# Optimization experiments

Measured on AMD Instinct MI355X. Metric: run time of the kernel, lower is better.

The kernel has to match this reference:

```python
import jax, jax.numpy as jnp
import numpy as np

N_NODES = 100000
N_EDGES = 6400000
ATOM_F = 128
R_CUT = 5.0


def setup_inputs() -> dict:
    key = jax.random.key(0)
    ks = jax.random.split(key, 9)
    x = jax.random.normal(ks[0], (N_NODES, ATOM_F), dtype=jnp.float32)
    rij = jax.random.uniform(ks[1], (N_EDGES,), dtype=jnp.float32) * R_CUT
    vij = jax.random.normal(ks[2], (N_EDGES, 3), dtype=jnp.float32)
    src = jax.random.randint(ks[3], (N_EDGES,), 0, N_NODES)
    dst = jax.random.randint(ks[4], (N_EDGES,), 0, N_NODES)
    # Dense params (PyTorch Linear default-ish init scale)
    s1 = 1.0 / np.sqrt(ATOM_F)
    W1 = jax.random.uniform(ks[5], (ATOM_F, ATOM_F), dtype=jnp.float32, minval=-s1, maxval=s1)
    b1 = jnp.zeros((ATOM_F,), dtype=jnp.float32)
    W2 = jax.random.uniform(ks[6], (ATOM_F, 1), dtype=jnp.float32, minval=-s1, maxval=s1)
    b2 = jnp.zeros((1,), dtype=jnp.float32)
    return {"x": x, "rij": rij, "vij": vij, "src": src, "dst": dst,
            "W1": W1, "b1": b1, "W2": W2, "b2": b2}


def reference(x, rij, vij, src, dst, W1, b1, W2, b2):
    # transform: Dense(F,F,swish) -> Dense(F,1,swish)
    h = jax.nn.silu(x @ W1 + b1)          # [N, F]
    q = jax.nn.silu(h @ W2 + b2)          # [N, 1]
    # cosine cutoff on edge distances
    c_ij = 0.5 * (jnp.cos(jnp.pi * rij / R_CUT) + 1.0)
    c_ij = c_ij * (rij < R_CUT).astype(rij.dtype)  # [E]
    # e_mul_u: broadcast source-node scalar onto edge vectors, scale by cutoff
    mu_ij = vij * q[src] * c_ij[:, None]  # [E, 3]
    # copy_e_sum: scatter-add edges into destination nodes
    mu = jax.ops.segment_sum(mu_ij, dst, num_segments=N_NODES)  # [N, 3]
    return mu
```

## Files before the change

### kernel.cpp

```cpp
#include <hip/hip_runtime.h>
#include <hip/hip_bf16.h>

#define NN 100000
#define NE 6400000
#define NSL 16
#define SLICE 6250
#define NB1 625
#define CHUNK (NE / NB1)
#define BCAP 840
#define C2 48
#define QSCALE 650.0f
#define QINV (1.0f / 650.0f)
#define QBIAS 5461

typedef __bf16 bf16x8_t __attribute__((ext_vector_type(8)));
typedef float f32x4_t __attribute__((ext_vector_type(4)));

__device__ __forceinline__ float silu_f(float v) { return v / (1.0f + __expf(-v)); }

__device__ __forceinline__ unsigned f16b(float v) {
    _Float16 h = (_Float16)v;
    unsigned short u;
    __builtin_memcpy(&u, &h, 2);
    return (unsigned)u;
}
__device__ __forceinline__ float f16f(unsigned u) {
    unsigned short us = (unsigned short)u;
    _Float16 h;
    __builtin_memcpy(&h, &us, 2);
    return (float)h;
}

__global__ __launch_bounds__(256, 2) void node_q_kernel(
    const float* __restrict__ x,
    const float* __restrict__ W1,
    const float* __restrict__ b1,
    const float* __restrict__ W2,
    const float* __restrict__ b2,
    float* __restrict__ q,
    int nGroups)
{
    __shared__ __align__(16) __bf16 w1s[2048 * 8];

    const int lane = threadIdx.x & 63;
    const int wave = threadIdx.x >> 6;
    const int c    = lane & 15;
    const int quad = lane >> 4;
    const int gwave  = blockIdx.x * 4 + wave;
    const int nWaves = gridDim.x * 4;

#pragma unroll
    for (int it = 0; it < 8; ++it) {
        const int e   = it * 256 + threadIdx.x;
        const int c_  = e & 15;
        const int nt_ = (e >> 4) & 7;
        const int qd  = (e >> 7) & 3;
        const int kt_ = e >> 9;
        const float* p = W1 + (kt_ * 32 + qd * 8) * 128 + nt_ * 16 + c_;
        bf16x8_t v;
#pragma unroll
        for (int j = 0; j < 8; ++j) v[j] = (__bf16)p[j * 128];
        *reinterpret_cast<bf16x8_t*>(&w1s[e * 8]) = v;
    }
    __syncthreads();

    bf16x8_t bfrag[8][4];
    float b1v[8], w2v[8];
#pragma unroll
    for (int nt = 0; nt < 8; ++nt) {
#pragma unroll
        for (int kt = 0; kt < 4; ++kt)
            bfrag[nt][kt] = *reinterpret_cast<const bf16x8_t*>(
                &w1s[(((kt * 4 + quad) * 8 + nt) * 16 + c) * 8]);
        b1v[nt] = b1[nt * 16 + c];
        w2v[nt] = W2[nt * 16 + c];
    }
    const float b2v = b2[0];

    for (int g = gwave; g < nGroups; g += nWaves) {
        const float* xrow = x + (size_t)(g * 16 + c) * 128 + quad * 8;
        bf16x8_t afrag[4];
#pragma unroll
        for (int kt = 0; kt < 4; ++kt) {
            const f32x4_t x0 = *reinterpret_cast<const f32x4_t*>(xrow + kt * 32);
            const f32x4_t x1 = *reinterpret_cast<const f32x4_t*>(xrow + kt * 32 + 4);
#pragma unroll
            for (int j = 0; j < 4; ++j) {
                afrag[kt][j]     = (__bf16)x0[j];
                afrag[kt][j + 4] = (__bf16)x1[j];
            }
        }

        float cr[4] = {0.f, 0.f, 0.f, 0.f};
#pragma unroll
        for (int nt = 0; nt < 8; ++nt) {
            f32x4_t acc = {0.f, 0.f, 0.f, 0.f};
#pragma unroll
            for (int kt = 0; kt < 4; ++kt)
                acc = __builtin_amdgcn_mfma_f32_16x16x32_bf16(afrag[kt], bfrag[nt][kt], acc, 0, 0, 0);
#pragma unroll
            for (int r = 0; r < 4; ++r)
                cr[r] += silu_f(acc[r] + b1v[nt]) * w2v[nt];
        }
#pragma unroll
        for (int r = 0; r < 4; ++r) {
            float v = cr[r];
            v += __shfl_xor(v, 1);
            v += __shfl_xor(v, 2);
            v += __shfl_xor(v, 4);
            v += __shfl_xor(v, 8);
            cr[r] = v;
        }
        if (c == 0) {
#pragma unroll
            for (int r = 0; r < 4; ++r)
                q[g * 16 + quad * 4 + r] = silu_f(cr[r] + b2v);
        }
    }
}

__global__ __launch_bounds__(256) void bucket_kernel(
    const float4* __restrict__ rij4,
    const float4* __restrict__ vij4,
    const int4* __restrict__ src4,
    const int4* __restrict__ dst4,
    const float* __restrict__ q,
    int* __restrict__ counts,
    uint2* __restrict__ arena)
{
    __shared__ int lcnt[NSL];
    const int t = threadIdx.x;
    const int lane = t & 63;
    if (t < NSL) lcnt[t] = 0;
    __syncthreads();

    const unsigned long long ltmask = (1ull << lane) - 1ull;
    const int g4 = blockIdx.x * (CHUNK / 4);
    const float K = 0.62831853071795864769f;

    for (int i = 0; i < CHUNK / 4 / 256; ++i) {
        const int idx = g4 + i * 256 + t;
        const int4 s = src4[idx];
        const int4 d = dst4[idx];
        const float4 r = rij4[idx];
        const float4 v0 = vij4[3 * idx + 0];
        const float4 v1 = vij4[3 * idx + 1];
        const float4 v2 = vij4[3 * idx + 2];

        const float c0 = (r.x < 5.0f) ? 0.5f * (__cosf(r.x * K) + 1.0f) : 0.0f;
        const float c1 = (r.y < 5.0f) ? 0.5f * (__cosf(r.y * K) + 1.0f) : 0.0f;
        const float c2 = (r.z < 5.0f) ? 0.5f * (__cosf(r.z * K) + 1.0f) : 0.0f;
        const float c3 = (r.w < 5.0f) ? 0.5f * (__cosf(r.w * K) + 1.0f) : 0.0f;
        const float w0 = q[s.x] * c0, w1 = q[s.y] * c1;
        const float w2 = q[s.z] * c2, w3 = q[s.w] * c3;

        int   dn[4] = {d.x, d.y, d.z, d.w};
        float px[4] = {v0.x * w0, v0.w * w1, v1.z * w2, v2.y * w3};
        float py[4] = {v0.y * w0, v1.x * w1, v1.w * w2, v2.z * w3};
        float pz[4] = {v0.z * w0, v1.y * w1, v2.x * w2, v2.w * w3};

#pragma unroll
        for (int j = 0; j < 4; ++j) {
            const int k  = dn[j] / SLICE;
            const int dl = dn[j] - k * SLICE;
            const float fx = fminf(fmaxf(px[j], -8.f), 8.f);
            const float fy = fminf(fmaxf(py[j], -8.f), 8.f);
            const float fz = fminf(fmaxf(pz[j], -8.f), 8.f);
            uint2 rec;
            rec.x = (unsigned)dl | (f16b(fx) << 16);
            rec.y = f16b(fy) | (f16b(fz) << 16);

            const unsigned long long b0 = __ballot(k & 1);
            const unsigned long long b1m = __ballot(k & 2);
            const unsigned long long b2m = __ballot(k & 4);
            const unsigned long long b3m = __ballot(k & 8);
            const unsigned long long eq =
                ((k & 1) ? b0 : ~b0) & ((k & 2) ? b1m : ~b1m) &
                ((k & 4) ? b2m : ~b2m) & ((k & 8) ? b3m : ~b3m);
            const int leader = __ffsll((long long)eq) - 1;
            const int rank   = __popcll(eq & ltmask);
            int base = 0;
            if (lane == leader) base = atomicAdd(&lcnt[k], __popcll(eq));
            base = __shfl(base, leader);
            const int pos = base + rank;
            if (pos < BCAP)
                arena[((size_t)k * NB1 + blockIdx.x) * BCAP + pos] = rec;
        }
    }
    __syncthreads();
    if (t < NSL) counts[blockIdx.x * NSL + t] = lcnt[t];
}

__global__ __launch_bounds__(256) void reduce_kernel(
    const uint2* __restrict__ arena,
    const int* __restrict__ counts,
    float* __restrict__ part)
{
    __shared__ unsigned long long acc[SLICE];
    const int s = blockIdx.x / C2;
    const int c = blockIdx.x % C2;

    for (int i = threadIdx.x; i < SLICE; i += 256) acc[i] = 0ull;
    __syncthreads();

    for (int b = c; b < NB1; b += C2) {
        const int n = counts[b * NSL + s];
        const uint2* seg = arena + ((size_t)s * NB1 + b) * BCAP;
        for (int i = threadIdx.x; i < n; i += 256) {
            const uint2 r = seg[i];
            const int node = r.x & 0xffffu;
            const int ix = __float2int_rn(f16f(r.x >> 16)      * QSCALE) + QBIAS;
            const int iy = __float2int_rn(f16f(r.y & 0xffffu)  * QSCALE) + QBIAS;
            const int iz = __float2int_rn(f16f(r.y >> 16)      * QSCALE) + QBIAS;
            const unsigned long long inc =
                (1ull << 54) |
                ((unsigned long long)(unsigned)ix << 36) |
                ((unsigned long long)(unsigned)iy << 18) |
                (unsigned long long)(unsigned)iz;
            atomicAdd(&acc[node], inc);
        }
    }
    __syncthreads();

    float* dp = part + (size_t)blockIdx.x * (SLICE * 3);
    for (int i = threadIdx.x; i < SLICE; i += 256) {
        const unsigned long long a = acc[i];
        const int cnt = (int)(a >> 54);
        const int X = (int)((a >> 36) & 0x3FFFFu) - cnt * QBIAS;
        const int Y = (int)((a >> 18) & 0x3FFFFu) - cnt * QBIAS;
        const int Z = (int)(a & 0x3FFFFu)         - cnt * QBIAS;
        dp[i * 3 + 0] = (float)X * QINV;
        dp[i * 3 + 1] = (float)Y * QINV;
        dp[i * 3 + 2] = (float)Z * QINV;
    }
}

__global__ __launch_bounds__(256) void finalize_kernel(
    const float* __restrict__ part,
    float* __restrict__ out)
{
    const int i = blockIdx.x * 256 + threadIdx.x;
    if (i >= NN * 3) return;
    const int n   = i / 3;
    const int k   = i - n * 3;
    const int s   = n / SLICE;
    const int l   = n - s * SLICE;
    const float* p = part + ((size_t)s * C2) * (SLICE * 3) + l * 3 + k;
    float sum = 0.f;
#pragma unroll
    for (int c = 0; c < C2; ++c) sum += p[(size_t)c * (SLICE * 3)];
    out[i] = sum;
}

__global__ __launch_bounds__(256) void edge_atomic_kernel(
    const float4* __restrict__ rij4,
    const float4* __restrict__ vij4,
    const int4* __restrict__ src4,
    const int4* __restrict__ dst4,
    const float* __restrict__ q,
    float* __restrict__ mu)
{
    const int t = blockIdx.x * 256 + threadIdx.x;
    const int4 s = src4[t];
    const int4 d = dst4[t];
    const float4 r = rij4[t];
    const float4 v0 = vij4[3 * t + 0];
    const float4 v1 = vij4[3 * t + 1];
    const float4 v2 = vij4[3 * t + 2];
    const float K = 0.62831853071795864769f;
    const float c0 = (r.x < 5.0f) ? 0.5f * (__cosf(r.x * K) + 1.0f) : 0.0f;
    const float c1 = (r.y < 5.0f) ? 0.5f * (__cosf(r.y * K) + 1.0f) : 0.0f;
    const float c2 = (r.z < 5.0f) ? 0.5f * (__cosf(r.z * K) + 1.0f) : 0.0f;
    const float c3 = (r.w < 5.0f) ? 0.5f * (__cosf(r.w * K) + 1.0f) : 0.0f;
    const float s0 = q[s.x] * c0, s1 = q[s.y] * c1, s2 = q[s.z] * c2, s3 = q[s.w] * c3;
    float* m0 = mu + 3 * (size_t)d.x;
    atomicAdd(m0 + 0, v0.x * s0); atomicAdd(m0 + 1, v0.y * s0); atomicAdd(m0 + 2, v0.z * s0);
    float* m1 = mu + 3 * (size_t)d.y;
    atomicAdd(m1 + 0, v0.w * s1); atomicAdd(m1 + 1, v1.x * s1); atomicAdd(m1 + 2, v1.y * s1);
    float* m2 = mu + 3 * (size_t)d.z;
    atomicAdd(m2 + 0, v1.z * s2); atomicAdd(m2 + 1, v1.w * s2); atomicAdd(m2 + 2, v2.x * s2);
    float* m3 = mu + 3 * (size_t)d.w;
    atomicAdd(m3 + 0, v2.y * s3); atomicAdd(m3 + 1, v2.z * s3); atomicAdd(m3 + 2, v2.w * s3);
}

extern "C" void kernel_launch(void* const* d_in, const int* in_sizes, int n_in,
                              void* d_out, int out_size, void* d_ws, size_t ws_size,
                              hipStream_t stream)
{
    const float* x   = (const float*)d_in[0];
    const float* rij = (const float*)d_in[1];
    const float* vij = (const float*)d_in[2];
    const int*   src = (const int*)d_in[3];
    const int*   dst = (const int*)d_in[4];
    const float* W1  = (const float*)d_in[5];
    const float* b1  = (const float*)d_in[6];
    const float* W2  = (const float*)d_in[7];
    const float* b2  = (const float*)d_in[8];

    char* ws = (char*)d_ws;
    const size_t Q_OFF    = 0;
    const size_t CNT_OFF  = 425984;
    const size_t REC_OFF  = 1048576;
    const size_t PART_OFF = REC_OFF + (size_t)NSL * NB1 * BCAP * 8;
    const size_t WS_NEEDED = PART_OFF + (size_t)NSL * C2 * SLICE * 3 * 4;

    float* q = (float*)(ws + Q_OFF);

    node_q_kernel<<<512, 256, 0, stream>>>(x, W1, b1, W2, b2, q, NN / 16);

    if (ws_size >= WS_NEEDED) {
        int*   counts = (int*)(ws + CNT_OFF);
        uint2* arena  = (uint2*)(ws + REC_OFF);
        float* part   = (float*)(ws + PART_OFF);

        bucket_kernel<<<NB1, 256, 0, stream>>>(
            (const float4*)rij, (const float4*)vij, (const int4*)src, (const int4*)dst,
            q, counts, arena);
        reduce_kernel<<<NSL * C2, 256, 0, stream>>>(arena, counts, part);
        finalize_kernel<<<(NN * 3 + 255) / 256, 256, 0, stream>>>(part, (float*)d_out);
    } else {
        hipMemsetAsync(d_out, 0, (size_t)NN * 3 * sizeof(float), stream);
        edge_atomic_kernel<<<NE / 4 / 256, 256, 0, stream>>>(
            (const float4*)rij, (const float4*)vij, (const int4*)src, (const int4*)dst,
            q, (float*)d_out);
    }
}
```

Measured before the change: 318.3 us.

## Stage bucketed edge records in LDS ring and flush in full wave-sized chunks

The bucketing kernel now collects per-slice records in a shared-memory ring buffer and writes them to global memory in contiguous 64-element chunks after each iteration, instead of scattering individual 8-byte stores to the arena. Block count doubles and per-bucket capacity shrinks to match. The aim is coalesced global writes at the cost of extra LDS traffic and two barriers per iteration. Residual records are compacted to the front of the ring, and the counts are clamped to capacity.

```diff
diff --git a/kernel.cpp b/kernel.cpp
--- a/kernel.cpp
+++ b/kernel.cpp
@@ -5,9 +5,10 @@
 #define NE 6400000
 #define NSL 16
 #define SLICE 6250
-#define NB1 625
+#define NB1 1250
 #define CHUNK (NE / NB1)
-#define BCAP 840
+#define BCAP 448
+#define CAPR 192
 #define C2 48
 #define QSCALE 650.0f
 #define QINV (1.0f / 650.0f)
@@ -128,10 +129,14 @@
     int* __restrict__ counts,
     uint2* __restrict__ arena)
 {
-    __shared__ int lcnt[NSL];
+    __shared__ uint2 ring[NSL][CAPR];
+    __shared__ int cnt[NSL];
+    __shared__ int gpos[NSL];
+
     const int t = threadIdx.x;
     const int lane = t & 63;
-    if (t < NSL) lcnt[t] = 0;
+    const int wave = t >> 6;
+    if (t < NSL) { cnt[t] = 0; gpos[t] = 0; }
     __syncthreads();
 
     const unsigned long long ltmask = (1ull << lane) - 1ull;
@@ -180,15 +185,42 @@
             const int leader = __ffsll((long long)eq) - 1;
             const int rank   = __popcll(eq & ltmask);
             int base = 0;
-            if (lane == leader) base = atomicAdd(&lcnt[k], __popcll(eq));
+            if (lane == leader) base = atomicAdd(&cnt[k], __popcll(eq));
             base = __shfl(base, leader);
             const int pos = base + rank;
-            if (pos < BCAP)
-                arena[((size_t)k * NB1 + blockIdx.x) * BCAP + pos] = rec;
-        }
-    }
-    __syncthreads();
-    if (t < NSL) counts[blockIdx.x * NSL + t] = lcnt[t];
+            if (pos < CAPR) ring[k][pos] = rec;
+        }
+        __syncthreads();
+
+        for (int sl = wave; sl < NSL; sl += 4) {
+            const int n = cnt[sl];
+            const int full = n & ~63;
+            if (full > 0) {
+                uint2* seg = arena + ((size_t)sl * NB1 + blockIdx.x) * BCAP + gpos[sl];
+                for (int off = 0; off + 64 <= n; off += 64) {
+                    const int p_ = gpos[sl] + off + lane;
+                    if (p_ < BCAP) seg[off + lane - 0] = ring[sl][off + lane];
+                }
+                const int resid = n - full;
+                uint2 keep;
+                if (lane < resid) keep = ring[sl][full + lane];
+                __builtin_amdgcn_s_waitcnt(0);
+                if (lane < resid) ring[sl][lane] = keep;
+                if (lane == 0) { gpos[sl] += full; cnt[sl] = resid; }
+            }
+        }
+        __syncthreads();
+    }
+
+    for (int sl = wave; sl < NSL; sl += 4) {
+        const int n = cnt[sl];
+        if (lane < n) {
+            const int p_ = gpos[sl] + lane;
+            if (p_ < BCAP)
+                arena[((size_t)sl * NB1 + blockIdx.x) * BCAP + p_] = ring[sl][lane];
+        }
+        if (lane == 0) counts[blockIdx.x * NSL + sl] = min(gpos[sl] + n, BCAP);
+    }
 }
 
 __global__ __launch_bounds__(256) void reduce_kernel(
```

New measurement: 288.7 us. 9.3% less time.
